# Performance work log

Measured on AMD Instinct MI355X. Metric: run time of the kernel, lower is better.

The kernel has to match this reference:

```python
import jax, jax.numpy as jnp
import numpy as np

B, F, NQ, DT, TS, K = 16384, 256, 2048, 256, 16, 8
GH, SH, CALH = 128, 128, 16
SPD = DT + TS
SPH = max(int(SPD * 0.25), 16)
CD = DT + 3 + TS + 3  # h_base + y_base + 3 gate stats + z_top + |d_safe| + |d_spec| = 278
CH = max(int(CD * 0.25), 16)
RES_SCALE = 0.1


def _ln(x, g, b):
    m = x.mean(-1, keepdims=True)
    v = ((x - m) ** 2).mean(-1, keepdims=True)
    return (x - m) * jax.lax.rsqrt(v + 1e-5) * g + b


def _resmlp(x, lg, lb, w1, b1, w2, b2):
    h = jnp.maximum(_ln(x, lg, lb) @ w1 + b1, 0.0)
    return h @ w2 + b2


def setup_inputs() -> dict:
    key = jax.random.key(0)
    ks = iter(jax.random.split(key, 48))
    def nrm(shape, s=0.05):
        return jax.random.normal(next(ks), shape, jnp.float32) * s
    d = {}
    d["x_num"] = jax.random.normal(next(ks), (B, F), jnp.float32)
    d["robust_center"] = nrm((1, F), 0.1)
    d["robust_scale"] = jax.random.uniform(next(ks), (1, F), jnp.float32, 0.5, 1.5)
    d["quantile_sorted"] = jnp.sort(jax.random.normal(next(ks), (NQ, F), jnp.float32), axis=0)
    d["stem_w1"] = nrm((3, CALH)); d["stem_b1"] = jnp.zeros((CALH,))
    d["stem_w2"] = nrm((CALH, CALH)); d["stem_b2"] = jnp.zeros((CALH,))
    d["stem_w3"] = nrm((CALH, 1)); d["stem_b3"] = jnp.zeros((1,))
    d["gate_w1"] = nrm((F, GH)); d["gate_b1"] = jnp.zeros((GH,))
    d["gate_w2"] = nrm((GH, F)); d["gate_b2"] = jnp.zeros((F,))
    d["bb_w"] = nrm((F, DT)); d["bb_b"] = jnp.zeros((DT,))
    d["base_w"] = nrm((DT, 1)); d["base_b"] = jnp.zeros((1,))
    d["safe_lg"] = jnp.ones((DT,)); d["safe_lb"] = jnp.zeros((DT,))
    d["safe_w1"] = nrm((DT, SH)); d["safe_b1"] = jnp.zeros((SH,))
    d["safe_w2"] = nrm((SH, 1)); d["safe_b2"] = jnp.zeros((1,))
    d["top_w1"] = nrm((1, TS)); d["top_b1"] = jnp.zeros((TS,))
    d["top_w2"] = nrm((TS, TS)); d["top_b2"] = jnp.zeros((TS,))
    d["spec_lg"] = jnp.ones((SPD,)); d["spec_lb"] = jnp.zeros((SPD,))
    d["spec_w1"] = nrm((SPD, SPH)); d["spec_b1"] = jnp.zeros((SPH,))
    d["spec_w2"] = nrm((SPH, 1)); d["spec_b2"] = jnp.zeros((1,))
    d["conf_lg"] = jnp.ones((CD,)); d["conf_lb"] = jnp.zeros((CD,))
    d["conf_w1"] = nrm((CD, CH)); d["conf_b1"] = jnp.zeros((CH,))
    d["conf_w2"] = nrm((CH, 1)); d["conf_b2"] = jnp.full((1,), -2.0)  # gamma_init_bias
    return d


def _forward(x_num, robust_center, robust_scale, quantile_sorted,
             stem_w1, stem_b1, stem_w2, stem_b2, stem_w3, stem_b3,
             gate_w1, gate_b1, gate_w2, gate_b2,
             bb_w, bb_b, base_w, base_b,
             safe_lg, safe_lb, safe_w1, safe_b1, safe_w2, safe_b2,
             top_w1, top_b1, top_w2, top_b2,
             spec_lg, spec_lb, spec_w1, spec_b1, spec_w2, spec_b2,
             conf_lg, conf_lb, conf_w1, conf_b1, conf_w2, conf_b2):
    # --- calibration views ---
    x_robust = (x_num - robust_center) / robust_scale
    ranks = jax.vmap(jnp.searchsorted, in_axes=(1, 1), out_axes=1)(
        jax.lax.stop_gradient(quantile_sorted), jax.lax.stop_gradient(x_num))  # [B,F] int
    x_quant = jnp.clip(ranks.astype(jnp.float32) / (NQ - 1.0), 0.0, 1.0)
    x_views = jnp.stack([x_num, x_robust, x_quant], axis=-1)  # [B,F,3]
    h = jnp.maximum(x_views @ stem_w1 + stem_b1, 0.0)
    h = jnp.maximum(h @ stem_w2 + stem_b2, 0.0)
    resid = jnp.tanh((h @ stem_w3 + stem_b3)[..., 0])
    x_cal = x_num + RES_SCALE * resid
    # --- input gate ---
    g = jax.nn.sigmoid(jnp.maximum(x_cal @ gate_w1 + gate_b1, 0.0) @ gate_w2 + gate_b2)
    x_gated = x_cal * g
    # --- backbone (stand-in for TMLPBackbone.encode_hidden) ---
    h_base = jnp.maximum(x_gated @ bb_w + bb_b, 0.0)  # [B,DT]
    y_base = h_base @ base_w + base_b  # [B,1]
    gate_mean = g.mean(axis=1, keepdims=True)
    gate_max = g.max(axis=1, keepdims=True)
    gate_std = g.std(axis=1, keepdims=True)  # ddof=0, matches unbiased=False
    delta_safe = _resmlp(h_base, safe_lg, safe_lb, safe_w1, safe_b1, safe_w2, safe_b2)
    # --- top-k feature gather ---
    topk_g, topk_idx = jax.lax.top_k(g, K)
    topk_x = jnp.take_along_axis(x_cal, topk_idx, axis=1)
    topk_w = topk_g / (topk_g.sum(axis=1, keepdims=True) + 1e-6)
    xw = (topk_x * topk_w)[..., None]  # [B,K,1]
    tok = jnp.maximum(xw @ top_w1 + top_b1, 0.0) @ top_w2 + top_b2  # [B,K,TS]
    z_top = tok.mean(axis=1)  # [B,TS]
    delta_spec = _resmlp(jnp.concatenate([h_base, z_top], axis=1),
                         spec_lg, spec_lb, spec_w1, spec_b1, spec_w2, spec_b2)
    conf_in = jnp.concatenate([h_base, y_base, gate_mean, gate_max, gate_std,
                               z_top, jnp.abs(delta_safe), jnp.abs(delta_spec)], axis=1)
    gamma = jax.nn.sigmoid(_resmlp(conf_in, conf_lg, conf_lb, conf_w1, conf_b1, conf_w2, conf_b2))
    return (y_base + delta_safe + gamma * delta_spec)[:, 0]


def reference(x_num, robust_center, robust_scale, quantile_sorted,
              stem_w1, stem_b1, stem_w2, stem_b2, stem_w3, stem_b3,
              gate_w1, gate_b1, gate_w2, gate_b2,
              bb_w, bb_b, base_w, base_b,
              safe_lg, safe_lb, safe_w1, safe_b1, safe_w2, safe_b2,
              top_w1, top_b1, top_w2, top_b2,
              spec_lg, spec_lb, spec_w1, spec_b1, spec_w2, spec_b2,
              conf_lg, conf_lb, conf_w1, conf_b1, conf_w2, conf_b2):
    return _forward(x_num, robust_center, robust_scale, quantile_sorted,
                    stem_w1, stem_b1, stem_w2, stem_b2, stem_w3, stem_b3,
                    gate_w1, gate_b1, gate_w2, gate_b2,
                    bb_w, bb_b, base_w, base_b,
                    safe_lg, safe_lb, safe_w1, safe_b1, safe_w2, safe_b2,
                    top_w1, top_b1, top_w2, top_b2,
                    spec_lg, spec_lb, spec_w1, spec_b1, spec_w2, spec_b2,
                    conf_lg, conf_lb, conf_w1, conf_b1, conf_w2, conf_b2)
```

## Files before the change

kernel.cpp:

```cpp
#include <hip/hip_runtime.h>
#include <math.h>

static constexpr int B  = 16384;
static constexpr int F  = 256;
static constexpr int NQ = 2048;
static constexpr int TS = 16;
static constexpr int KTOP = 8;
static constexpr int SPD = 272;
static constexpr int SPH = 68;
static constexpr int CD  = 278;
static constexpr int CH  = 69;

typedef __attribute__((ext_vector_type(8))) short bf16x8;
typedef __attribute__((ext_vector_type(4))) float f32x4;
typedef _Float16 f16x2 __attribute__((ext_vector_type(2)));

__device__ inline short f2bf(float f) {
    unsigned u = __builtin_bit_cast(unsigned, f);
    unsigned r = (u + 0x7FFF + ((u >> 16) & 1)) >> 16;
    return (short)r;
}

__device__ inline float fast_tanh(float o) {
    o = fminf(fmaxf(o, -15.0f), 15.0f);
    float e = __expf(2.0f * o);
    return (e - 1.0f) / (e + 1.0f);
}

__device__ inline f16x2 cvt2h(float a, float b) {
    return __builtin_bit_cast(f16x2, __builtin_amdgcn_cvt_pkrtz(a, b));
}

__device__ inline unsigned pack2h(float a, float b) {
    return __builtin_bit_cast(unsigned, __builtin_amdgcn_cvt_pkrtz(a, b));
}

__device__ inline void prep_one(const float* W, short* T, int local,
                                int K, int N, int KP) {
    const int n = local / KP, k = local - n * KP;
    T[local] = (k < K && n < N) ? f2bf(W[k * N + n]) : (short)0;
}

__global__ __launch_bounds__(256) void k_prepall(
    const float* __restrict__ gate_w1, const float* __restrict__ gate_w2,
    const float* __restrict__ bb_w,    const float* __restrict__ safe_w1,
    const float* __restrict__ spec_w1, const float* __restrict__ conf_w1,
    const float* __restrict__ qs,
    const float* __restrict__ stem_w2, const float* __restrict__ stem_w3,
    short* __restrict__ w1t, short* __restrict__ w2t, short* __restrict__ bbt,
    short* __restrict__ sw1t, short* __restrict__ spw1t, short* __restrict__ cfw1t,
    float* __restrict__ qs_t,
    unsigned* __restrict__ w2ph, unsigned* __restrict__ w3ph)
{
    const int idx = blockIdx.x * 256 + threadIdx.x;
    if (idx < 32768)       prep_one(gate_w1, w1t,  idx,           256, 128, 256);
    else if (idx < 65536)  prep_one(gate_w2, w2t,  idx - 32768,   128, 256, 128);
    else if (idx < 131072) prep_one(bb_w,    bbt,  idx - 65536,   256, 256, 256);
    else if (idx < 163840) prep_one(safe_w1, sw1t, idx - 131072,  256, 128, 256);
    else if (idx < 200704) prep_one(spec_w1, spw1t, idx - 163840, 272, 68, 288);
    else if (idx < 237568) prep_one(conf_w1, cfw1t, idx - 200704, 278, 69, 288);
    else if (idx < 761856) {
        const int local = idx - 237568;
        const int f = local >> 11, q = local & 2047;
        qs_t[local] = qs[q * 256 + f];
    }
    else if (idx < 761984) {
        const int l = idx - 761856;
        const int t = l >> 4, j = l & 15;
        w2ph[l] = pack2h(stem_w2[(2 * t) * 16 + j], stem_w2[(2 * t + 1) * 16 + j]);
    }
    else if (idx < 761992) {
        const int u = idx - 761984;
        w3ph[u] = pack2h(stem_w3[2 * u], stem_w3[2 * u + 1]);
    }
}

__global__ __launch_bounds__(256) void k_calib7(
    const float* __restrict__ x_num, const float* __restrict__ center,
    const float* __restrict__ scale, const float* __restrict__ qs,
    const float* __restrict__ qs_t,
    const float* __restrict__ sw1, const float* __restrict__ sb1,
    const unsigned* __restrict__ w2ph, const float* __restrict__ sb2,
    const unsigned* __restrict__ w3ph, const float* __restrict__ sb3,
    float* __restrict__ x_cal)
{
    __shared__ float cq[63 * 256];
    const int tid = threadIdx.x;
    const int f = tid;
#pragma unroll 1
    for (int j = 0; j < 63; ++j)
        cq[j * 256 + tid] = qs[(32 * (j + 1)) * 256 + tid];
    __syncthreads();

    const float c = center[f];
    const float inv_sc = 1.0f / scale[f];
    const float* colp = qs_t + (long)f * NQ;
    const long row_base = (long)blockIdx.x * 32;

    float xb[8];
#pragma unroll
    for (int i = 0; i < 8; ++i) xb[i] = x_num[(row_base + i) * F + f];

#pragma unroll 1
    for (int grp = 0; grp < 4; ++grp) {
        const long r0 = row_base + grp * 8;
        float x[8], xr[8];
#pragma unroll
        for (int i = 0; i < 8; ++i) x[i] = xb[i];
        if (grp < 3) {
#pragma unroll
            for (int i = 0; i < 8; ++i) xb[i] = x_num[(r0 + 8 + i) * F + f];
        }
#pragma unroll
        for (int i = 0; i < 8; ++i) xr[i] = (x[i] - c) * inv_sc;

        int lo[8], hi[8];
#pragma unroll
        for (int i = 0; i < 8; ++i) { lo[i] = 0; hi[i] = 63; }
#pragma unroll
        for (int it = 0; it < 6; ++it) {
            float qv[8]; int mid[8];
#pragma unroll
            for (int i = 0; i < 8; ++i) {
                mid[i] = (lo[i] + hi[i]) >> 1;
                qv[i] = cq[mid[i] * 256 + f];
            }
#pragma unroll
            for (int i = 0; i < 8; ++i) {
                if (qv[i] < x[i]) lo[i] = mid[i] + 1; else hi[i] = mid[i];
            }
        }
        int base[8];
        {
            float pm[8];
#pragma unroll
            for (int i = 0; i < 8; ++i) pm[i] = colp[lo[i] * 32 + 16];
#pragma unroll
            for (int i = 0; i < 8; ++i)
                base[i] = lo[i] * 32 + ((pm[i] < x[i]) ? 16 : 0);
        }
        float xq[8];
#pragma unroll
        for (int i = 0; i < 8; ++i) {
            const float4* wp = reinterpret_cast<const float4*>(&colp[base[i]]);
            const float4 a = wp[0], b = wp[1], d = wp[2], e = wp[3];
            int cN = 0;
            cN += (a.x < x[i]); cN += (a.y < x[i]); cN += (a.z < x[i]); cN += (a.w < x[i]);
            cN += (b.x < x[i]); cN += (b.y < x[i]); cN += (b.z < x[i]); cN += (b.w < x[i]);
            cN += (d.x < x[i]); cN += (d.y < x[i]); cN += (d.z < x[i]); cN += (d.w < x[i]);
            cN += (e.x < x[i]); cN += (e.y < x[i]); cN += (e.z < x[i]); cN += (e.w < x[i]);
            const int rank = base[i] + cN;
            xq[i] = fminf((float)rank * (1.0f / (float)(NQ - 1)), 1.0f);
        }

#pragma unroll
        for (int hgrp = 0; hgrp < 2; ++hgrp) {
            const int o4 = hgrp * 4;
            float h2[4][16];
#pragma unroll
            for (int j = 0; j < 16; ++j) {
                const float bb = sb2[j];
#pragma unroll
                for (int i = 0; i < 4; ++i) h2[i][j] = bb;
            }
#pragma unroll 4
            for (int t = 0; t < 8; ++t) {
                const float w0a = sw1[2 * t],     w1a = sw1[16 + 2 * t],     w2a = sw1[32 + 2 * t];
                const float w0b = sw1[2 * t + 1], w1b = sw1[16 + 2 * t + 1], w2b = sw1[32 + 2 * t + 1];
                const float ba = sb1[2 * t], bbv = sb1[2 * t + 1];
                f16x2 hp[4];
#pragma unroll
                for (int i = 0; i < 4; ++i) {
                    const float ha = fmaxf(ba  + x[o4 + i] * w0a + xr[o4 + i] * w1a + xq[o4 + i] * w2a, 0.0f);
                    const float hb = fmaxf(bbv + x[o4 + i] * w0b + xr[o4 + i] * w1b + xq[o4 + i] * w2b, 0.0f);
                    hp[i] = cvt2h(ha, hb);
                }
                unsigned ww[16];
                const uint4* wr = reinterpret_cast<const uint4*>(&w2ph[t * 16]);
                *reinterpret_cast<uint4*>(&ww[0])  = wr[0];
                *reinterpret_cast<uint4*>(&ww[4])  = wr[1];
                *reinterpret_cast<uint4*>(&ww[8])  = wr[2];
                *reinterpret_cast<uint4*>(&ww[12]) = wr[3];
#pragma unroll
                for (int j = 0; j < 16; ++j) {
                    const f16x2 wj = __builtin_bit_cast(f16x2, ww[j]);
#pragma unroll
                    for (int i = 0; i < 4; ++i)
                        h2[i][j] = __builtin_amdgcn_fdot2(hp[i], wj, h2[i][j], false);
                }
            }
            const float b3 = sb3[0];
            float o[4] = {b3, b3, b3, b3};
#pragma unroll
            for (int u = 0; u < 8; ++u) {
                const f16x2 wu = __builtin_bit_cast(f16x2, w3ph[u]);
#pragma unroll
                for (int i = 0; i < 4; ++i) {
                    const f16x2 hh = cvt2h(
                        fmaxf(h2[i][2 * u], 0.0f), fmaxf(h2[i][2 * u + 1], 0.0f));
                    o[i] = __builtin_amdgcn_fdot2(hh, wu, o[i], false);
                }
            }
#pragma unroll
            for (int i = 0; i < 4; ++i)
                x_cal[(r0 + o4 + i) * F + f] = x[o4 + i] + 0.1f * fast_tanh(o[i]);
        }
    }
}

static constexpr int ST1 = 136;
static constexpr int ST2 = 264;

__global__ __launch_bounds__(256) void k_fused(
    const float* __restrict__ x_cal,
    const short* __restrict__ w1t, const float* __restrict__ gate_b1,
    const short* __restrict__ w2t, const float* __restrict__ gate_b2,
    const short* __restrict__ bbt, const float* __restrict__ bb_b,
    float* __restrict__ g, float* __restrict__ h_b)
{
    __shared__ short s_c1[32 * ST1];
    __shared__ short s_xg[32 * ST2];

    const int tid = threadIdx.x;
    const int wave = tid >> 6, lane = tid & 63;
    const int sub = lane & 15, quad = lane >> 4;
    const int wm = wave & 1, wn = wave >> 1;
    const long row0 = (long)blockIdx.x * 32;
    const long mrow = row0 + wm * 16 + sub;

    {
        f32x4 acc[4];
#pragma unroll
        for (int t = 0; t < 4; ++t) acc[t] = (f32x4){0, 0, 0, 0};
#pragma unroll
        for (int k0 = 0; k0 < 256; k0 += 32) {
            const float* ap = x_cal + mrow * 256 + k0 + quad * 8;
            float av[8];
            *reinterpret_cast<float4*>(&av[0]) = *reinterpret_cast<const float4*>(ap);
            *reinterpret_cast<float4*>(&av[4]) = *reinterpret_cast<const float4*>(ap + 4);
            bf16x8 af;
#pragma unroll
            for (int j = 0; j < 8; ++j) af[j] = f2bf(av[j]);
#pragma unroll
            for (int t = 0; t < 4; ++t) {
                const int col = wn * 64 + t * 16 + sub;
                const bf16x8 bf = *reinterpret_cast<const bf16x8*>(
                    &w1t[(long)col * 256 + k0 + quad * 8]);
                acc[t] = __builtin_amdgcn_mfma_f32_16x16x32_bf16(af, bf, acc[t], 0, 0, 0);
            }
        }
#pragma unroll
        for (int t = 0; t < 4; ++t) {
            const int col = wn * 64 + t * 16 + sub;
            const float bb = gate_b1[col];
#pragma unroll
            for (int r = 0; r < 4; ++r) {
                const int rowl = wm * 16 + quad * 4 + r;
                s_c1[rowl * ST1 + col] = f2bf(fmaxf(acc[t][r] + bb, 0.0f));
            }
        }
    }
    __syncthreads();

    {
        f32x4 acc[8];
#pragma unroll
        for (int t = 0; t < 8; ++t) acc[t] = (f32x4){0, 0, 0, 0};
#pragma unroll
        for (int k0 = 0; k0 < 128; k0 += 32) {
            const bf16x8 af = *reinterpret_cast<const bf16x8*>(
                &s_c1[(wm * 16 + sub) * ST1 + k0 + quad * 8]);
#pragma unroll
            for (int t = 0; t < 8; ++t) {
                const int col = wn * 128 + t * 16 + sub;
                const bf16x8 bf = *reinterpret_cast<const bf16x8*>(
                    &w2t[(long)col * 128 + k0 + quad * 8]);
                acc[t] = __builtin_amdgcn_mfma_f32_16x16x32_bf16(af, bf, acc[t], 0, 0, 0);
            }
        }
#pragma unroll
        for (int t = 0; t < 8; ++t) {
            const int col = wn * 128 + t * 16 + sub;
            const float bb = gate_b2[col];
#pragma unroll
            for (int r = 0; r < 4; ++r) {
                const int rowl = wm * 16 + quad * 4 + r;
                const float gv = 1.0f / (1.0f + __expf(-(acc[t][r] + bb)));
                g[(row0 + rowl) * 256 + col] = gv;
                const float xg = x_cal[(row0 + rowl) * 256 + col] * gv;
                s_xg[rowl * ST2 + col] = f2bf(xg);
            }
        }
    }
    __syncthreads();

    {
        f32x4 acc[8];
#pragma unroll
        for (int t = 0; t < 8; ++t) acc[t] = (f32x4){0, 0, 0, 0};
#pragma unroll
        for (int k0 = 0; k0 < 256; k0 += 32) {
            const bf16x8 af = *reinterpret_cast<const bf16x8*>(
                &s_xg[(wm * 16 + sub) * ST2 + k0 + quad * 8]);
#pragma unroll
            for (int t = 0; t < 8; ++t) {
                const int col = wn * 128 + t * 16 + sub;
                const bf16x8 bf = *reinterpret_cast<const bf16x8*>(
                    &bbt[(long)col * 256 + k0 + quad * 8]);
                acc[t] = __builtin_amdgcn_mfma_f32_16x16x32_bf16(af, bf, acc[t], 0, 0, 0);
            }
        }
#pragma unroll
        for (int t = 0; t < 8; ++t) {
            const int col = wn * 128 + t * 16 + sub;
            const float bb = bb_b[col];
#pragma unroll
            for (int r = 0; r < 4; ++r) {
                const int rowl = wm * 16 + quad * 4 + r;
                h_b[(row0 + rowl) * 256 + col] = fmaxf(acc[t][r] + bb, 0.0f);
            }
        }
    }
}

__global__ __launch_bounds__(64) void k_topk(
    const float* __restrict__ g, const float* __restrict__ x_cal,
    const float* __restrict__ tw1, const float* __restrict__ tb1,
    const float* __restrict__ tw2, const float* __restrict__ tb2,
    float* __restrict__ z_top, float* __restrict__ stats)
{
    __shared__ float s_hm[16];
    const int b = blockIdx.x;
    const int lane = threadIdx.x;
    const long base = (long)b * F;

    float gv[4];
#pragma unroll
    for (int i = 0; i < 4; ++i) gv[i] = g[base + lane + 64 * i];

    float s = gv[0] + gv[1] + gv[2] + gv[3];
    float mx = fmaxf(fmaxf(gv[0], gv[1]), fmaxf(gv[2], gv[3]));
    for (int m = 32; m; m >>= 1) {
        s  += __shfl_xor(s, m);
        mx  = fmaxf(mx, __shfl_xor(mx, m));
    }
    const float mean = s * (1.0f / 256.0f);
    float vs = 0.0f;
#pragma unroll
    for (int i = 0; i < 4; ++i) { float d = gv[i] - mean; vs += d * d; }
    for (int m = 32; m; m >>= 1) vs += __shfl_xor(vs, m);
    const float stdv = sqrtf(vs * (1.0f / 256.0f));

    float cur[4]; int curi[4];
#pragma unroll
    for (int i = 0; i < 4; ++i) { cur[i] = gv[i]; curi[i] = lane + 64 * i; }
    float tv[KTOP]; int ti[KTOP]; float vsum = 0.0f;
    for (int r = 0; r < KTOP; ++r) {
        float bv = cur[0]; int bi = curi[0];
#pragma unroll
        for (int i = 1; i < 4; ++i)
            if (cur[i] > bv || (cur[i] == bv && curi[i] < bi)) { bv = cur[i]; bi = curi[i]; }
        for (int m = 32; m; m >>= 1) {
            float ov = __shfl_xor(bv, m);
            int   oi = __shfl_xor(bi, m);
            if (ov > bv || (ov == bv && oi < bi)) { bv = ov; bi = oi; }
        }
        tv[r] = bv; ti[r] = bi; vsum += bv;
#pragma unroll
        for (int i = 0; i < 4; ++i) if (curi[i] == bi) cur[i] = -INFINITY;
    }
    const float denom = 1.0f / (vsum + 1e-6f);

    if (lane < 16) {
        float hm = 0.0f;
        for (int k = 0; k < KTOP; ++k) {
            const float xk = x_cal[base + ti[k]];
            const float xw = xk * (tv[k] * denom);
            hm += fmaxf(xw * tw1[lane] + tb1[lane], 0.0f);
        }
        s_hm[lane] = hm * (1.0f / (float)KTOP);
    }
    __syncthreads();
    if (lane < 16) {
        float z = tb2[lane];
#pragma unroll
        for (int j = 0; j < 16; ++j) z += s_hm[j] * tw2[j * 16 + lane];
        z_top[(long)b * TS + lane] = z;
    }
    if (lane == 0) {
        stats[(long)b * 4 + 0] = mean;
        stats[(long)b * 4 + 1] = mx;
        stats[(long)b * 4 + 2] = stdv;
    }
}

static constexpr int HST = 260;
static constexpr int AST = 312;

template<int KP>
__device__ __forceinline__ void head_mfma16(
    const short* sa, const short* __restrict__ Wt,
    const float* __restrict__ b1v, const float* __restrict__ w2v, int Nreal,
    float (*s_red)[16], int wave, int sub, int quad)
{
    f32x4 acc[2];
#pragma unroll
    for (int t = 0; t < 2; ++t) acc[t] = (f32x4){0, 0, 0, 0};
#pragma unroll
    for (int k0 = 0; k0 < KP; k0 += 32) {
        const bf16x8 af = *reinterpret_cast<const bf16x8*>(
            &sa[sub * AST + k0 + quad * 8]);
#pragma unroll
        for (int t = 0; t < 2; ++t) {
            const int col = wave * 32 + t * 16 + sub;
            const bf16x8 bf = *reinterpret_cast<const bf16x8*>(
                &Wt[(long)col * KP + k0 + quad * 8]);
            acc[t] = __builtin_amdgcn_mfma_f32_16x16x32_bf16(af, bf, acc[t], 0, 0, 0);
        }
    }
    float rsum[4] = {0, 0, 0, 0};
#pragma unroll
    for (int t = 0; t < 2; ++t) {
        const int col = wave * 32 + t * 16 + sub;
        const float bb = (col < Nreal) ? b1v[col] : 0.0f;
        const float ww = (col < Nreal) ? w2v[col] : 0.0f;
#pragma unroll
        for (int rr = 0; rr < 4; ++rr)
            rsum[rr] += fmaxf(acc[t][rr] + bb, 0.0f) * ww;
    }
#pragma unroll
    for (int rr = 0; rr < 4; ++rr)
        for (int m = 1; m < 16; m <<= 1) rsum[rr] += __shfl_xor(rsum[rr], m);
    if (sub == 0) {
#pragma unroll
        for (int rr = 0; rr < 4; ++rr)
            s_red[wave][quad * 4 + rr] = rsum[rr];
    }
}

__global__ __launch_bounds__(256) void k_tail3(
    const float* __restrict__ h_base, const float* __restrict__ z_top,
    const float* __restrict__ gstats,
    const float* __restrict__ base_w, const float* __restrict__ base_b,
    const float* __restrict__ safe_lg, const float* __restrict__ safe_lb,
    const short* __restrict__ sw1t, const float* __restrict__ safe_b1,
    const float* __restrict__ safe_w2, const float* __restrict__ safe_b2,
    const float* __restrict__ spec_lg, const float* __restrict__ spec_lb,
    const short* __restrict__ spw1t, const float* __restrict__ spec_b1,
    const float* __restrict__ spec_w2, const float* __restrict__ spec_b2,
    const float* __restrict__ conf_lg, const float* __restrict__ conf_lb,
    const short* __restrict__ cfw1t, const float* __restrict__ conf_b1,
    const float* __restrict__ conf_w2, const float* __restrict__ conf_b2,
    float* __restrict__ out)
{
    __shared__ float s_h[16 * HST];
    __shared__ short s_a[16 * AST];
    __shared__ float s_z[16 * 16];
    __shared__ float s_g[16 * 4];
    __shared__ float s_sc[16 * 14];
    __shared__ float s_red[4][16];

    const int tid = threadIdx.x;
    const int wave = tid >> 6, lane = tid & 63;
    const int sub = lane & 15, quad = lane >> 4;
    const long row0 = (long)blockIdx.x * 16;

    for (int idx = tid; idx < 16 * 64; idx += 256) {
        const int r = idx >> 6, q = idx & 63;
        *reinterpret_cast<float4*>(&s_h[r * HST + q * 4]) =
            *reinterpret_cast<const float4*>(&h_base[(row0 + r) * 256 + q * 4]);
    }
    if (tid < 256) s_z[tid] = z_top[row0 * 16 + tid];
    if (tid < 64) s_g[tid] = gstats[row0 * 4 + tid];
    __syncthreads();

    {
        const int r = tid >> 4, l16 = tid & 15;
        float S = 0.0f, SS = 0.0f, Y = 0.0f;
#pragma unroll
        for (int i = 0; i < 16; ++i) {
            const int k = l16 + 16 * i;
            const float v = s_h[r * HST + k];
            S += v; SS += v * v; Y += v * base_w[k];
        }
        const float z0 = s_z[r * 16 + l16];
        float Sz = z0, SSz = z0 * z0;
#pragma unroll
        for (int m = 1; m < 16; m <<= 1) {
            S += __shfl_xor(S, m); SS += __shfl_xor(SS, m); Y += __shfl_xor(Y, m);
            Sz += __shfl_xor(Sz, m); SSz += __shfl_xor(SSz, m);
        }
        if (l16 == 0) {
            float* sc = &s_sc[r * 14];
            sc[0] = S; sc[1] = SS; sc[2] = Sz; sc[3] = SSz;
            sc[4] = Y + base_b[0];
            const float mu = S * (1.0f / 256.0f);
            sc[5] = mu;
            sc[6] = rsqrtf(SS * (1.0f / 256.0f) - mu * mu + 1e-5f);
            const float musp = (S + Sz) * (1.0f / (float)SPD);
            sc[7] = musp;
            sc[8] = rsqrtf((SS + SSz) * (1.0f / (float)SPD) - musp * musp + 1e-5f);
        }
    }
    __syncthreads();

    for (int idx = tid; idx < 16 * 128; idx += 256) {
        const int r = idx >> 7, k = (idx & 127) * 2;
        const float mu = s_sc[r * 14 + 5], rs = s_sc[r * 14 + 6];
        const float v0 = (s_h[r * HST + k] - mu) * rs * safe_lg[k] + safe_lb[k];
        const float v1 = (s_h[r * HST + k + 1] - mu) * rs * safe_lg[k + 1] + safe_lb[k + 1];
        const unsigned pk = (unsigned)(unsigned short)f2bf(v0) |
                            ((unsigned)(unsigned short)f2bf(v1) << 16);
        *reinterpret_cast<unsigned*>(&s_a[r * AST + k]) = pk;
    }
    __syncthreads();

    head_mfma16<256>(s_a, sw1t, safe_b1, safe_w2, 128, s_red, wave, sub, quad);
    __syncthreads();

    if (tid < 16)
        s_sc[tid * 14 + 9] = s_red[0][tid] + s_red[1][tid] + s_red[2][tid] + s_red[3][tid] + safe_b2[0];
    for (int idx = tid; idx < 16 * 144; idx += 256) {
        const int r = idx / 144, k = (idx - r * 144) * 2;
        const float mu = s_sc[r * 14 + 7], rs = s_sc[r * 14 + 8];
        float vv[2];
#pragma unroll
        for (int h = 0; h < 2; ++h) {
            const int kk = k + h;
            float raw = (kk < 256) ? s_h[r * HST + kk]
                       : (kk < SPD) ? s_z[r * 16 + kk - 256] : 0.0f;
            vv[h] = (kk < SPD) ? (raw - mu) * rs * spec_lg[kk] + spec_lb[kk] : 0.0f;
        }
        const unsigned pk = (unsigned)(unsigned short)f2bf(vv[0]) |
                            ((unsigned)(unsigned short)f2bf(vv[1]) << 16);
        *reinterpret_cast<unsigned*>(&s_a[r * AST + k]) = pk;
    }
    __syncthreads();

    head_mfma16<288>(s_a, spw1t, spec_b1, spec_w2, SPH, s_red, wave, sub, quad);
    __syncthreads();

    if (tid < 16) {
        float* sc = &s_sc[tid * 14];
        const float dsp = s_red[0][tid] + s_red[1][tid] + s_red[2][tid] + s_red[3][tid] + spec_b2[0];
        sc[10] = dsp;
        const float yb = sc[4];
        const float gm = s_g[tid * 4 + 0], gx = s_g[tid * 4 + 1], gs = s_g[tid * 4 + 2];
        const float ads = fabsf(sc[9]), adp = fabsf(dsp);
        const float es = yb + gm + gx + gs + ads + adp;
        const float eq = yb * yb + gm * gm + gx * gx + gs * gs + ads * ads + adp * adp;
        const float muc = (sc[0] + sc[2] + es) * (1.0f / (float)CD);
        sc[11] = muc;
        sc[12] = rsqrtf((sc[1] + sc[3] + eq) * (1.0f / (float)CD) - muc * muc + 1e-5f);
    }
    __syncthreads();

    for (int idx = tid; idx < 16 * 144; idx += 256) {
        const int r = idx / 144, k = (idx - r * 144) * 2;
        const float mu = s_sc[r * 14 + 11], rs = s_sc[r * 14 + 12];
        float vv[2];
#pragma unroll
        for (int h = 0; h < 2; ++h) {
            const int kk = k + h;
            float raw;
            if (kk < 256)       raw = s_h[r * HST + kk];
            else if (kk == 256) raw = s_sc[r * 14 + 4];
            else if (kk == 257) raw = s_g[r * 4 + 0];
            else if (kk == 258) raw = s_g[r * 4 + 1];
            else if (kk == 259) raw = s_g[r * 4 + 2];
            else if (kk < 276)  raw = s_z[r * 16 + kk - 260];
            else if (kk == 276) raw = fabsf(s_sc[r * 14 + 9]);
            else if (kk == 277) raw = fabsf(s_sc[r * 14 + 10]);
            else                raw = 0.0f;
            vv[h] = (kk < CD) ? (raw - mu) * rs * conf_lg[kk] + conf_lb[kk] : 0.0f;
        }
        const unsigned pk = (unsigned)(unsigned short)f2bf(vv[0]) |
                            ((unsigned)(unsigned short)f2bf(vv[1]) << 16);
        *reinterpret_cast<unsigned*>(&s_a[r * AST + k]) = pk;
    }
    __syncthreads();

    head_mfma16<288>(s_a, cfw1t, conf_b1, conf_w2, CH, s_red, wave, sub, quad);
    __syncthreads();

    if (tid < 16) {
        const float* sc = &s_sc[tid * 14];
        const float gamma = 1.0f / (1.0f + __expf(
            -(s_red[0][tid] + s_red[1][tid] + s_red[2][tid] + s_red[3][tid] + conf_b2[0])));
        out[row0 + tid] = sc[4] + sc[9] + gamma * sc[10];
    }
}

extern "C" void kernel_launch(void* const* d_in, const int* in_sizes, int n_in,
                              void* d_out, int out_size, void* d_ws, size_t ws_size,
                              hipStream_t stream)
{
    const float* x_num   = (const float*)d_in[0];
    const float* center  = (const float*)d_in[1];
    const float* scale   = (const float*)d_in[2];
    const float* qs      = (const float*)d_in[3];
    const float* stem_w1 = (const float*)d_in[4];
    const float* stem_b1 = (const float*)d_in[5];
    const float* stem_w2 = (const float*)d_in[6];
    const float* stem_b2 = (const float*)d_in[7];
    const float* stem_w3 = (const float*)d_in[8];
    const float* stem_b3 = (const float*)d_in[9];
    const float* gate_w1 = (const float*)d_in[10];
    const float* gate_b1 = (const float*)d_in[11];
    const float* gate_w2 = (const float*)d_in[12];
    const float* gate_b2 = (const float*)d_in[13];
    const float* bb_w    = (const float*)d_in[14];
    const float* bb_b    = (const float*)d_in[15];
    const float* base_w  = (const float*)d_in[16];
    const float* base_b  = (const float*)d_in[17];
    const float* safe_lg = (const float*)d_in[18];
    const float* safe_lb = (const float*)d_in[19];
    const float* safe_w1 = (const float*)d_in[20];
    const float* safe_b1 = (const float*)d_in[21];
    const float* safe_w2 = (const float*)d_in[22];
    const float* safe_b2 = (const float*)d_in[23];
    const float* top_w1  = (const float*)d_in[24];
    const float* top_b1  = (const float*)d_in[25];
    const float* top_w2  = (const float*)d_in[26];
    const float* top_b2  = (const float*)d_in[27];
    const float* spec_lg = (const float*)d_in[28];
    const float* spec_lb = (const float*)d_in[29];
    const float* spec_w1 = (const float*)d_in[30];
    const float* spec_b1 = (const float*)d_in[31];
    const float* spec_w2 = (const float*)d_in[32];
    const float* spec_b2 = (const float*)d_in[33];
    const float* conf_lg = (const float*)d_in[34];
    const float* conf_lb = (const float*)d_in[35];
    const float* conf_w1 = (const float*)d_in[36];
    const float* conf_b1 = (const float*)d_in[37];
    const float* conf_w2 = (const float*)d_in[38];
    const float* conf_b2 = (const float*)d_in[39];

    float* ws    = (float*)d_ws;
    float* x_cal = ws;
    float* g_h   = x_cal + (long)B * 256;
    float* g     = g_h   + (long)B * 128;
    float* h_b   = g     + (long)B * 256;
    float* z_top = h_b   + (long)B * 256;
    float* gstat = z_top + (long)B * 16;
    short* w1t   = (short*)(gstat + (long)B * 4);
    short* w2t   = w1t   + 128 * 256;
    short* bbt   = w2t   + 256 * 128;
    short* sw1t  = bbt   + 256 * 256;
    short* spw1t = sw1t  + 128 * 256;
    short* cfw1t = spw1t + 128 * 288;
    unsigned* w2ph = (unsigned*)(cfw1t + 128 * 288);
    unsigned* w3ph = w2ph + 128;
    float* qs_t  = h_b;
    float* out   = (float*)d_out;

    k_prepall<<<2977, 256, 0, stream>>>(gate_w1, gate_w2, bb_w, safe_w1, spec_w1,
                                        conf_w1, qs, stem_w2, stem_w3,
                                        w1t, w2t, bbt, sw1t, spw1t, cfw1t, qs_t,
                                        w2ph, w3ph);
    k_calib7<<<512, 256, 0, stream>>>(x_num, center, scale, qs, qs_t,
                                      stem_w1, stem_b1, w2ph, stem_b2, w3ph, stem_b3,
                                      x_cal);
    k_fused<<<512, 256, 0, stream>>>(x_cal, w1t, gate_b1, w2t, gate_b2, bbt, bb_b,
                                     g, h_b);
    k_topk<<<B, 64, 0, stream>>>(g, x_cal, top_w1, top_b1, top_w2, top_b2, z_top, gstat);
    k_tail3<<<B / 16, 256, 0, stream>>>(h_b, z_top, gstat,
                                        base_w, base_b,
                                        safe_lg, safe_lb, sw1t, safe_b1, safe_w2, safe_b2,
                                        spec_lg, spec_lb, spw1t, spec_b1, spec_w2, spec_b2,
                                        conf_lg, conf_lb, cfw1t, conf_b1, conf_w2, conf_b2,
                                        out);
}
```

Before: 307.8 us.

## Pack bf16 conversions, batch quantile preload, and group top-k rows per block

Replaces the manual per-element bf16 rounding with packed float2-to-bfloat162 conversions in the gate GEMM and the tail heads, which should shorten the conversion instruction sequences. The calibration kernel now issues its quantile-column preload in batches of nine independent loads before the shared-memory stores, exposing more memory-level parallelism. The top-k kernel handles four rows per 256-thread block instead of one row per 64-thread block, which cuts the block count and scheduling overhead. Each wave now also waits at a block-wide barrier for the other three waves. Packed conversion may treat NaN differently from the old bit-twiddling rounding.

```diff
diff --git a/kernel.cpp b/kernel.cpp
--- a/kernel.cpp
+++ b/kernel.cpp
@@ -1,4 +1,5 @@
 #include <hip/hip_runtime.h>
+#include <hip/hip_bf16.h>
 #include <math.h>
 
 static constexpr int B  = 16384;
@@ -14,11 +15,19 @@
 typedef __attribute__((ext_vector_type(8))) short bf16x8;
 typedef __attribute__((ext_vector_type(4))) float f32x4;
 typedef _Float16 f16x2 __attribute__((ext_vector_type(2)));
+typedef unsigned u32x4 __attribute__((ext_vector_type(4)));
 
 __device__ inline short f2bf(float f) {
     unsigned u = __builtin_bit_cast(unsigned, f);
     unsigned r = (u + 0x7FFF + ((u >> 16) & 1)) >> 16;
     return (short)r;
+}
+
+__device__ inline unsigned pkbf(float a, float b) {
+    __hip_bfloat162 h = __float22bfloat162_rn(make_float2(a, b));
+    unsigned u;
+    __builtin_memcpy(&u, &h, 4);
+    return u;
 }
 
 __device__ inline float fast_tanh(float o) {
@@ -88,8 +97,13 @@
     const int tid = threadIdx.x;
     const int f = tid;
 #pragma unroll 1
-    for (int j = 0; j < 63; ++j)
-        cq[j * 256 + tid] = qs[(32 * (j + 1)) * 256 + tid];
+    for (int j0 = 0; j0 < 63; j0 += 9) {
+        float t[9];
+#pragma unroll
+        for (int u = 0; u < 9; ++u) t[u] = qs[(32 * (j0 + u + 1)) * 256 + tid];
+#pragma unroll
+        for (int u = 0; u < 9; ++u) cq[(j0 + u) * 256 + tid] = t[u];
+    }
     __syncthreads();
 
     const float c = center[f];
@@ -238,9 +252,12 @@
             float av[8];
             *reinterpret_cast<float4*>(&av[0]) = *reinterpret_cast<const float4*>(ap);
             *reinterpret_cast<float4*>(&av[4]) = *reinterpret_cast<const float4*>(ap + 4);
-            bf16x8 af;
-#pragma unroll
-            for (int j = 0; j < 8; ++j) af[j] = f2bf(av[j]);
+            u32x4 afu;
+            afu[0] = pkbf(av[0], av[1]);
+            afu[1] = pkbf(av[2], av[3]);
+            afu[2] = pkbf(av[4], av[5]);
+            afu[3] = pkbf(av[6], av[7]);
+            const bf16x8 af = __builtin_bit_cast(bf16x8, afu);
 #pragma unroll
             for (int t = 0; t < 4; ++t) {
                 const int col = wn * 64 + t * 16 + sub;
@@ -323,15 +340,16 @@
     }
 }
 
-__global__ __launch_bounds__(64) void k_topk(
+__global__ __launch_bounds__(256) void k_topk(
     const float* __restrict__ g, const float* __restrict__ x_cal,
     const float* __restrict__ tw1, const float* __restrict__ tb1,
     const float* __restrict__ tw2, const float* __restrict__ tb2,
     float* __restrict__ z_top, float* __restrict__ stats)
 {
-    __shared__ float s_hm[16];
-    const int b = blockIdx.x;
-    const int lane = threadIdx.x;
+    __shared__ float s_hm[4][16];
+    const int wave = threadIdx.x >> 6;
+    const int lane = threadIdx.x & 63;
+    const int b = blockIdx.x * 4 + wave;
     const long base = (long)b * F;
 
     float gv[4];
@@ -378,13 +396,13 @@
             const float xw = xk * (tv[k] * denom);
             hm += fmaxf(xw * tw1[lane] + tb1[lane], 0.0f);
         }
-        s_hm[lane] = hm * (1.0f / (float)KTOP);
+        s_hm[wave][lane] = hm * (1.0f / (float)KTOP);
     }
     __syncthreads();
     if (lane < 16) {
         float z = tb2[lane];
 #pragma unroll
-        for (int j = 0; j < 16; ++j) z += s_hm[j] * tw2[j * 16 + lane];
+        for (int j = 0; j < 16; ++j) z += s_hm[wave][j] * tw2[j * 16 + lane];
         z_top[(long)b * TS + lane] = z;
     }
     if (lane == 0) {
@@ -509,9 +527,7 @@
         const float mu = s_sc[r * 14 + 5], rs = s_sc[r * 14 + 6];
         const float v0 = (s_h[r * HST + k] - mu) * rs * safe_lg[k] + safe_lb[k];
         const float v1 = (s_h[r * HST + k + 1] - mu) * rs * safe_lg[k + 1] + safe_lb[k + 1];
-        const unsigned pk = (unsigned)(unsigned short)f2bf(v0) |
-                            ((unsigned)(unsigned short)f2bf(v1) << 16);
-        *reinterpret_cast<unsigned*>(&s_a[r * AST + k]) = pk;
+        *reinterpret_cast<unsigned*>(&s_a[r * AST + k]) = pkbf(v0, v1);
     }
     __syncthreads();
 
@@ -531,9 +547,7 @@
                        : (kk < SPD) ? s_z[r * 16 + kk - 256] : 0.0f;
             vv[h] = (kk < SPD) ? (raw - mu) * rs * spec_lg[kk] + spec_lb[kk] : 0.0f;
         }
-        const unsigned pk = (unsigned)(unsigned short)f2bf(vv[0]) |
-                            ((unsigned)(unsigned short)f2bf(vv[1]) << 16);
-        *reinterpret_cast<unsigned*>(&s_a[r * AST + k]) = pk;
+        *reinterpret_cast<unsigned*>(&s_a[r * AST + k]) = pkbf(vv[0], vv[1]);
     }
     __syncthreads();
 
@@ -574,9 +588,7 @@
             else                raw = 0.0f;
             vv[h] = (kk < CD) ? (raw - mu) * rs * conf_lg[kk] + conf_lb[kk] : 0.0f;
         }
-        const unsigned pk = (unsigned)(unsigned short)f2bf(vv[0]) |
-                            ((unsigned)(unsigned short)f2bf(vv[1]) << 16);
-        *reinterpret_cast<unsigned*>(&s_a[r * AST + k]) = pk;
+        *reinterpret_cast<unsigned*>(&s_a[r * AST + k]) = pkbf(vv[0], vv[1]);
     }
     __syncthreads();
 
@@ -663,7 +675,7 @@
                                       x_cal);
     k_fused<<<512, 256, 0, stream>>>(x_cal, w1t, gate_b1, w2t, gate_b2, bbt, bb_b,
                                      g, h_b);
-    k_topk<<<B, 64, 0, stream>>>(g, x_cal, top_w1, top_b1, top_w2, top_b2, z_top, gstat);
+    k_topk<<<B / 4, 256, 0, stream>>>(g, x_cal, top_w1, top_b1, top_w2, top_b2, z_top, gstat);
     k_tail3<<<B / 16, 256, 0, stream>>>(h_b, z_top, gstat,
                                         base_w, base_b,
                                         safe_lg, safe_lb, sw1t, safe_b1, safe_w2, safe_b2,
```

After: 306.5 us. About the same (-0.4%).
